# Kernel optimization log

Hardware: AMD Instinct MI355X
Metric: run time of the kernel (lower is better)

The kernel has to match this reference:

```python
import jax, jax.numpy as jnp
import numpy as np

EPS = 1e-8  # torch.cosine_similarity eps
TEMPERATURE = 1.0


def setup_inputs() -> dict:
    key = jax.random.key(0)
    ks = jax.random.split(key, 12)
    B = 16384
    inp = {
        "user_ids": jax.random.randint(ks[0], (B, 8), 0, 100000),
        "item_ids": jax.random.randint(ks[1], (B, 4), 0, 50000),
        "sample_weight": jax.random.uniform(ks[2], (B,), jnp.float32, 0.01, 1.0),
        "user_table": jax.random.normal(ks[3], (100000, 64), jnp.float32) * 0.05,
        "item_table": jax.random.normal(ks[4], (50000, 64), jnp.float32) * 0.05,
        "uW1": jax.random.normal(ks[5], (512, 256), jnp.float32) * 0.04,
        "ub1": jnp.zeros((256,), jnp.float32),
        "uW2": jax.random.normal(ks[6], (256, 128), jnp.float32) * 0.06,
        "ub2": jnp.zeros((128,), jnp.float32),
        "iW1": jax.random.normal(ks[7], (256, 256), jnp.float32) * 0.06,
        "ib1": jnp.zeros((256,), jnp.float32),
        "iW2": jax.random.normal(ks[8], (256, 128), jnp.float32) * 0.06,
        "ib2": jnp.zeros((128,), jnp.float32),
        "n_neg": 3,
    }
    return inp


def _tower(ids, table, W1, b1, W2, b2):
    # embedding lookup [B, F, D] -> concat -> [B, F*D], then 2-layer relu MLP
    B = ids.shape[0]
    e = table[ids].reshape(B, -1)
    h = jax.nn.relu(e @ W1 + b1)
    return jax.nn.relu(h @ W2 + b2)


def reference(user_ids, item_ids, sample_weight, user_table, item_table,
              uW1, ub1, uW2, ub2, iW1, ib1, iW2, ib2, n_neg):
    u = _tower(user_ids, user_table, uW1, ub1, uW2, ub2)  # [B, 128]
    v = _tower(item_ids, item_table, iW1, ib1, iW2, ib2)  # [B, 128]
    # cosine similarity per row (torch eps clamp on norms)
    un = jnp.maximum(jnp.linalg.norm(u, axis=1), EPS)
    vn = jnp.maximum(jnp.linalg.norm(v, axis=1), EPS)
    y = jnp.sum(u * v, axis=1) / (un * vn)
    # sampling-bias correction
    y = y - jnp.log(sample_weight)
    # vectorized wrap-around in-batch negative gather:
    # scores[i] = [y[i], y[(i+1)%B], ..., y[(i+n_neg)%B]]
    B = y.shape[0]
    idx = (jnp.arange(B)[:, None] + jnp.arange(n_neg + 1)[None, :]) % B
    scores = y[idx] / TEMPERATURE  # [B, 1+n_neg]
    return scores
```

## Files before the change

### kernel.cpp

```cpp
#include <hip/hip_runtime.h>
#include <math.h>

#define CEPS 1e-8f

typedef __attribute__((ext_vector_type(8))) short bf16x8;
typedef __attribute__((ext_vector_type(4))) float f32x4;
typedef __attribute__((ext_vector_type(4))) unsigned int u32x4;

__device__ __forceinline__ unsigned short f2bf(float f) {
    unsigned u = __builtin_bit_cast(unsigned, f);
    u += 0x7fffu + ((u >> 16) & 1u);
    return (unsigned short)(u >> 16);
}

__global__ __launch_bounds__(256)
void pack_all(const float* __restrict__ uW1, const float* __restrict__ uW2,
              const float* __restrict__ iW1, const float* __restrict__ iW2,
              unsigned short* __restrict__ o1, unsigned short* __restrict__ o2,
              unsigned short* __restrict__ o3, unsigned short* __restrict__ o4)
{
    int g = blockIdx.x * 256 + threadIdx.x;
    const float* src; unsigned short* dst; int N; int base;
    if (g < 16384)      { src = uW1; dst = o1; N = 256; base = 0;     }
    else if (g < 20480) { src = uW2; dst = o2; N = 128; base = 16384; }
    else if (g < 28672) { src = iW1; dst = o3; N = 256; base = 20480; }
    else                { src = iW2; dst = o4; N = 128; base = 28672; }
    int i = g - base;
    int kg = i / N, n = i - kg * N;
    unsigned short tmp[8];
    #pragma unroll
    for (int j = 0; j < 8; ++j)
        tmp[j] = f2bf(src[(kg * 8 + j) * N + n]);
    *reinterpret_cast<bf16x8*>(dst + ((size_t)i << 3)) =
        *reinterpret_cast<bf16x8*>(tmp);
}


template<int F>
__device__ __forceinline__ void stage_emb(const int* __restrict__ ids,
                                          const float* __restrict__ table,
                                          unsigned short* e_s, int row0, int tid)
{
    constexpr int FC = F * 8;
    constexpr int IT = (64 * FC) / 1024;
    int idv[IT];
    #pragma unroll
    for (int it = 0; it < IT; ++it) {
        int c = tid + it * 1024;
        int r = c / FC, f = (c % FC) >> 3;
        idv[it] = ids[(row0 + r) * F + f];
    }
    #pragma unroll
    for (int it = 0; it < IT; ++it) {
        int c = tid + it * 1024;
        int r = c / FC, rem = c % FC, ci = rem & 7;
        const float* src = table + (size_t)idv[it] * 64 + ci * 8;
        float4 aa = *reinterpret_cast<const float4*>(src);
        float4 bb = *reinterpret_cast<const float4*>(src + 4);
        u32x4 pk;
        pk.x = f2bf(aa.x) | ((unsigned)f2bf(aa.y) << 16);
        pk.y = f2bf(aa.z) | ((unsigned)f2bf(aa.w) << 16);
        pk.z = f2bf(bb.x) | ((unsigned)f2bf(bb.y) << 16);
        pk.w = f2bf(bb.z) | ((unsigned)f2bf(bb.w) << 16);
        int byte = r * (F * 128) + rem * 16;
        byte ^= (r & 7) << 4;
        *reinterpret_cast<u32x4*>(reinterpret_cast<char*>(e_s) + byte) = pk;
    }
}

template<int KB>
__device__ __forceinline__ bf16x8 loadA(const unsigned short* s, int ks, int m,
                                        int l15, int l4)
{
    int row = m * 16 + l15;
    int byte = row * (KB * 2) + ks * 64 + l4 * 16;
    byte ^= (row & 7) << 4;
    return *reinterpret_cast<const bf16x8*>(
               reinterpret_cast<const char*>(s) + byte);
}

template<int K1>
__device__ __forceinline__ void gemm1(
    const unsigned short* e_s, unsigned short* h_s,
    const unsigned short* __restrict__ W1p, const float* __restrict__ b1,
    int l15, int l4, int wl, const bf16x8* b0)
{
    constexpr int NKS = K1 / 32;
    const int colbase = wl * 32;
    f32x4 acc[4][2];
    #pragma unroll
    for (int m = 0; m < 4; ++m)
        #pragma unroll
        for (int n = 0; n < 2; ++n) acc[m][n] = (f32x4){0.f, 0.f, 0.f, 0.f};

    const unsigned short* Wbase = W1p + (((l4 * 256) + colbase + l15) << 3);
    bf16x8 aB[2][4], bB[2][2];
    bB[0][0] = b0[0];
    bB[0][1] = b0[1];
    #pragma unroll
    for (int m = 0; m < 4; ++m) aB[0][m] = loadA<K1>(e_s, 0, m, l15, l4);

    #pragma unroll
    for (int ks = 0; ks < NKS; ++ks) {
        const int cur = ks & 1, nxt = cur ^ 1;
        if (ks + 1 < NKS) {
            #pragma unroll
            for (int m = 0; m < 4; ++m)
                aB[nxt][m] = loadA<K1>(e_s, ks + 1, m, l15, l4);
            #pragma unroll
            for (int n = 0; n < 2; ++n)
                bB[nxt][n] = *reinterpret_cast<const bf16x8*>(
                                 Wbase + (ks + 1) * 8192 + (n << 7));
        }
        #pragma unroll
        for (int n = 0; n < 2; ++n)
            #pragma unroll
            for (int m = 0; m < 4; ++m)
                acc[m][n] = __builtin_amdgcn_mfma_f32_16x16x32_bf16(
                                aB[cur][m], bB[cur][n], acc[m][n], 0, 0, 0);
    }
    #pragma unroll
    for (int n = 0; n < 2; ++n) {
        int col = colbase + n * 16 + l15;
        float bias = b1[col];
        #pragma unroll
        for (int m = 0; m < 4; ++m)
            #pragma unroll
            for (int r = 0; r < 4; ++r) {
                int row = m * 16 + l4 * 4 + r;
                float v = acc[m][n][r] + bias;
                v = v > 0.f ? v : 0.f;
                int byte = (row * 256 + col) * 2;
                byte ^= (row & 7) << 4;
                *reinterpret_cast<unsigned short*>(
                    reinterpret_cast<char*>(h_s) + byte) = f2bf(v);
            }
    }
}

__device__ __forceinline__ void gemm2(
    const unsigned short* h_s, const unsigned short* __restrict__ W2p,
    f32x4 (&acc)[4], int l15, int l4, int wl, bf16x8 b0)
{
    const int col = wl * 16 + l15;
    #pragma unroll
    for (int m = 0; m < 4; ++m) acc[m] = (f32x4){0.f, 0.f, 0.f, 0.f};

    const unsigned short* Wbase = W2p + (((l4 * 128) + col) << 3);
    bf16x8 aB[2][4], bB[2];
    bB[0] = b0;
    #pragma unroll
    for (int m = 0; m < 4; ++m) aB[0][m] = loadA<256>(h_s, 0, m, l15, l4);

    #pragma unroll
    for (int ks = 0; ks < 8; ++ks) {
        const int cur = ks & 1, nxt = cur ^ 1;
        if (ks + 1 < 8) {
            #pragma unroll
            for (int m = 0; m < 4; ++m)
                aB[nxt][m] = loadA<256>(h_s, ks + 1, m, l15, l4);
            bB[nxt] = *reinterpret_cast<const bf16x8*>(Wbase + (ks + 1) * 4096);
        }
        #pragma unroll
        for (int m = 0; m < 4; ++m)
            acc[m] = __builtin_amdgcn_mfma_f32_16x16x32_bf16(
                         aB[cur][m], bB[cur], acc[m], 0, 0, 0);
    }
}

__global__ __launch_bounds__(1024)
void fused_sbc(const int* __restrict__ user_ids,  const int* __restrict__ item_ids,
               const float* __restrict__ user_table, const float* __restrict__ item_table,
               const unsigned short* __restrict__ uW1p, const float* __restrict__ ub1,
               const unsigned short* __restrict__ uW2p, const float* __restrict__ ub2,
               const unsigned short* __restrict__ iW1p, const float* __restrict__ ib1,
               const unsigned short* __restrict__ iW2p, const float* __restrict__ ib2,
               const float* __restrict__ sw, float* __restrict__ out,
               int B, int nn1)
{
    __shared__ __align__(16) unsigned short smem[81920];
    unsigned short* e_u = smem;
    unsigned short* e_i = smem + 32768;
    unsigned short* h_u = smem + 49152;
    unsigned short* h_i = smem + 65536;
    float* V_lds = reinterpret_cast<float*>(smem);
    float* red   = reinterpret_cast<float*>(smem + 32768);

    const int tid  = threadIdx.x;
    const int lane = tid & 63;
    const int w    = tid >> 6;
    const int l15  = lane & 15, l4 = lane >> 4;
    const int role = w >> 3;
    const int wl   = w & 7;
    const int row0 = blockIdx.x * 64;

    const unsigned short* W1sel = role ? iW1p : uW1p;
    const unsigned short* W2sel = role ? iW2p : uW2p;

    bf16x8 b0g1[2];
    {
        const unsigned short* base = W1sel + ((l4 * 256 + wl * 32 + l15) << 3);
        b0g1[0] = *reinterpret_cast<const bf16x8*>(base);
        b0g1[1] = *reinterpret_cast<const bf16x8*>(base + 128);
    }
    stage_emb<8>(user_ids, user_table, e_u, row0, tid);
    stage_emb<4>(item_ids, item_table, e_i, row0, tid);
    __syncthreads();

    if (role == 0) gemm1<512>(e_u, h_u, uW1p, ub1, l15, l4, wl, b0g1);
    else           gemm1<256>(e_i, h_i, iW1p, ib1, l15, l4, wl, b0g1);
    bf16x8 b0g2 = *reinterpret_cast<const bf16x8*>(
                      W2sel + ((l4 * 128 + wl * 16 + l15) << 3));
    __syncthreads();

    f32x4 acc2[4];
    if (role == 0) gemm2(h_u, uW2p, acc2, l15, l4, wl, b0g2);
    else           gemm2(h_i, iW2p, acc2, l15, l4, wl, b0g2);

    const int col = wl * 16 + l15;

    if (role == 1) {
        const float bv = ib2[col];
        float pv[16];
        #pragma unroll
        for (int m = 0; m < 4; ++m)
            #pragma unroll
            for (int r = 0; r < 4; ++r) {
                float vv = acc2[m][r] + bv;
                vv = vv > 0.f ? vv : 0.f;
                int row = m * 16 + l4 * 4 + r;
                V_lds[row * 132 + col] = vv;
                pv[m * 4 + r] = vv * vv;
            }
        #pragma unroll
        for (int off = 1; off < 16; off <<= 1)
            #pragma unroll
            for (int i = 0; i < 16; ++i)
                pv[i] += __shfl_xor(pv[i], off);
        if (l15 == 0) {
            #pragma unroll
            for (int m = 0; m < 4; ++m)
                #pragma unroll
                for (int r = 0; r < 4; ++r) {
                    int row = m * 16 + l4 * 4 + r;
                    red[(wl * 64 + row) * 3 + 2] = pv[m * 4 + r];
                }
        }
    }
    __syncthreads();

    if (role == 0) {
        const float bu = ub2[col];
        float pd[16], pu[16];
        #pragma unroll
        for (int m = 0; m < 4; ++m)
            #pragma unroll
            for (int r = 0; r < 4; ++r) {
                float uu = acc2[m][r] + bu;
                uu = uu > 0.f ? uu : 0.f;
                int row = m * 16 + l4 * 4 + r;
                float vv = V_lds[row * 132 + col];
                pd[m * 4 + r] = uu * vv;
                pu[m * 4 + r] = uu * uu;
            }
        #pragma unroll
        for (int off = 1; off < 16; off <<= 1)
            #pragma unroll
            for (int i = 0; i < 16; ++i) {
                pd[i] += __shfl_xor(pd[i], off);
                pu[i] += __shfl_xor(pu[i], off);
            }
        if (l15 == 0) {
            #pragma unroll
            for (int m = 0; m < 4; ++m)
                #pragma unroll
                for (int r = 0; r < 4; ++r) {
                    int row = m * 16 + l4 * 4 + r;
                    red[(wl * 64 + row) * 3 + 0] = pd[m * 4 + r];
                    red[(wl * 64 + row) * 3 + 1] = pu[m * 4 + r];
                }
        }
    }
    __syncthreads();

    if (tid < 64) {
        int row = tid;
        float d = 0.f, su = 0.f, sv = 0.f;
        #pragma unroll
        for (int cg = 0; cg < 8; ++cg) {
            d  += red[(cg * 64 + row) * 3 + 0];
            su += red[(cg * 64 + row) * 3 + 1];
            sv += red[(cg * 64 + row) * 3 + 2];
        }
        float un = fmaxf(sqrtf(su), CEPS);
        float vn = fmaxf(sqrtf(sv), CEPS);
        int grow = row0 + row;
        float yv = d / (un * vn) - logf(sw[grow]);
        for (int j = 0; j < nn1; ++j) {
            int idx = grow - j;
            if (idx < 0) idx += B;
            out[idx * nn1 + j] = yv;
        }
    }
}

extern "C" void kernel_launch(void* const* d_in, const int* in_sizes, int n_in,
                              void* d_out, int out_size, void* d_ws, size_t ws_size,
                              hipStream_t stream)
{
    const int*   user_ids   = (const int*)  d_in[0];
    const int*   item_ids   = (const int*)  d_in[1];
    const float* sw         = (const float*)d_in[2];
    const float* user_table = (const float*)d_in[3];
    const float* item_table = (const float*)d_in[4];
    const float* uW1        = (const float*)d_in[5];
    const float* ub1        = (const float*)d_in[6];
    const float* uW2        = (const float*)d_in[7];
    const float* ub2        = (const float*)d_in[8];
    const float* iW1        = (const float*)d_in[9];
    const float* ib1        = (const float*)d_in[10];
    const float* iW2        = (const float*)d_in[11];
    const float* ib2        = (const float*)d_in[12];

    const int B   = in_sizes[2];
    const int nn1 = out_size / B;

    unsigned short* wp   = (unsigned short*)d_ws;
    unsigned short* uW1p = wp;
    unsigned short* uW2p = wp + 131072;
    unsigned short* iW1p = wp + 163840;
    unsigned short* iW2p = wp + 229376;
    float* out = (float*)d_out;

    pack_all<<<128, 256, 0, stream>>>(uW1, uW2, iW1, iW2,
                                      uW1p, uW2p, iW1p, iW2p);
    fused_sbc<<<B / 64, 1024, 0, stream>>>(user_ids, item_ids,
                                           user_table, item_table,
                                           uW1p, ub1, uW2p, ub2,
                                           iW1p, ib1, iW2p, ib2,
                                           sw, out, B, nn1);
}
```

Measured before the change: 32.40 us.

## Swap MFMA operand roles, triple-buffer weight loads, vectorize epilogue reductions

Weights now feed the MFMA A operand and activations the B operand, so each lane's accumulator holds 4 consecutive output columns of one row. This lets the bias/ReLU epilogue write packed 8-byte bf16 stores and cuts the cosine reductions from 4-step 16-wide shuffles over 16 values to 2 shuffles over 4 values. Global weight fragments are prefetched two k-steps ahead with a 3-slot ring, MFMA blocks run under raised s_setprio, and launch bounds ask for 4 waves per SIMD. The V staging stride drops to 129. Risks are register pressure from the deeper prefetch under the tighter launch bound, and possible LDS bank conflicts in the new store pattern.

Result: faster. 28.56 us (-11.8%).

```diff
diff --git a/kernel.cpp b/kernel.cpp
--- a/kernel.cpp
+++ b/kernel.cpp
@@ -6,6 +6,7 @@
 typedef __attribute__((ext_vector_type(8))) short bf16x8;
 typedef __attribute__((ext_vector_type(4))) float f32x4;
 typedef __attribute__((ext_vector_type(4))) unsigned int u32x4;
+typedef __attribute__((ext_vector_type(2))) unsigned int u32x2;
 
 __device__ __forceinline__ unsigned short f2bf(float f) {
     unsigned u = __builtin_bit_cast(unsigned, f);
@@ -53,8 +54,8 @@
     #pragma unroll
     for (int it = 0; it < IT; ++it) {
         int c = tid + it * 1024;
-        int r = c / FC, rem = c % FC, ci = rem & 7;
-        const float* src = table + (size_t)idv[it] * 64 + ci * 8;
+        int r = c / FC, rem = c % FC;
+        const float* src = table + (size_t)idv[it] * 64 + (rem & 7) * 8;
         float4 aa = *reinterpret_cast<const float4*>(src);
         float4 bb = *reinterpret_cast<const float4*>(src + 4);
         u32x4 pk;
@@ -69,10 +70,10 @@
 }
 
 template<int KB>
-__device__ __forceinline__ bf16x8 loadA(const unsigned short* s, int ks, int m,
+__device__ __forceinline__ bf16x8 loadA(const unsigned short* s, int ks, int ni,
                                         int l15, int l4)
 {
-    int row = m * 16 + l15;
+    int row = ni * 16 + l15;
     int byte = row * (KB * 2) + ks * 64 + l4 * 16;
     byte ^= (row & 7) << 4;
     return *reinterpret_cast<const bf16x8*>(
@@ -83,92 +84,105 @@
 __device__ __forceinline__ void gemm1(
     const unsigned short* e_s, unsigned short* h_s,
     const unsigned short* __restrict__ W1p, const float* __restrict__ b1,
-    int l15, int l4, int wl, const bf16x8* b0)
+    int l15, int l4, int wl, const bf16x8* w0)
 {
     constexpr int NKS = K1 / 32;
-    const int colbase = wl * 32;
-    f32x4 acc[4][2];
-    #pragma unroll
-    for (int m = 0; m < 4; ++m)
-        #pragma unroll
-        for (int n = 0; n < 2; ++n) acc[m][n] = (f32x4){0.f, 0.f, 0.f, 0.f};
-
-    const unsigned short* Wbase = W1p + (((l4 * 256) + colbase + l15) << 3);
-    bf16x8 aB[2][4], bB[2][2];
-    bB[0][0] = b0[0];
-    bB[0][1] = b0[1];
-    #pragma unroll
-    for (int m = 0; m < 4; ++m) aB[0][m] = loadA<K1>(e_s, 0, m, l15, l4);
+    f32x4 acc[2][4];
+    #pragma unroll
+    for (int mi = 0; mi < 2; ++mi)
+        #pragma unroll
+        for (int ni = 0; ni < 4; ++ni) acc[mi][ni] = (f32x4){0.f, 0.f, 0.f, 0.f};
+
+    const unsigned short* Wbase = W1p + ((l4 * 256 + wl * 32 + l15) << 3);
+    bf16x8 wf[3][2], ef[2][4];
+    wf[0][0] = w0[0];
+    wf[0][1] = w0[1];
+    #pragma unroll
+    for (int mi = 0; mi < 2; ++mi)
+        wf[1][mi] = *reinterpret_cast<const bf16x8*>(Wbase + 8192 + (mi << 7));
+    #pragma unroll
+    for (int ni = 0; ni < 4; ++ni) ef[0][ni] = loadA<K1>(e_s, 0, ni, l15, l4);
 
     #pragma unroll
     for (int ks = 0; ks < NKS; ++ks) {
-        const int cur = ks & 1, nxt = cur ^ 1;
+        if (ks + 2 < NKS) {
+            #pragma unroll
+            for (int mi = 0; mi < 2; ++mi)
+                wf[(ks + 2) % 3][mi] = *reinterpret_cast<const bf16x8*>(
+                    Wbase + (ks + 2) * 8192 + (mi << 7));
+        }
         if (ks + 1 < NKS) {
             #pragma unroll
-            for (int m = 0; m < 4; ++m)
-                aB[nxt][m] = loadA<K1>(e_s, ks + 1, m, l15, l4);
-            #pragma unroll
-            for (int n = 0; n < 2; ++n)
-                bB[nxt][n] = *reinterpret_cast<const bf16x8*>(
-                                 Wbase + (ks + 1) * 8192 + (n << 7));
-        }
-        #pragma unroll
-        for (int n = 0; n < 2; ++n)
-            #pragma unroll
-            for (int m = 0; m < 4; ++m)
-                acc[m][n] = __builtin_amdgcn_mfma_f32_16x16x32_bf16(
-                                aB[cur][m], bB[cur][n], acc[m][n], 0, 0, 0);
-    }
-    #pragma unroll
-    for (int n = 0; n < 2; ++n) {
-        int col = colbase + n * 16 + l15;
-        float bias = b1[col];
-        #pragma unroll
-        for (int m = 0; m < 4; ++m)
-            #pragma unroll
-            for (int r = 0; r < 4; ++r) {
-                int row = m * 16 + l4 * 4 + r;
-                float v = acc[m][n][r] + bias;
-                v = v > 0.f ? v : 0.f;
-                int byte = (row * 256 + col) * 2;
-                byte ^= (row & 7) << 4;
-                *reinterpret_cast<unsigned short*>(
-                    reinterpret_cast<char*>(h_s) + byte) = f2bf(v);
-            }
+            for (int ni = 0; ni < 4; ++ni)
+                ef[(ks + 1) & 1][ni] = loadA<K1>(e_s, ks + 1, ni, l15, l4);
+        }
+        __builtin_amdgcn_s_setprio(1);
+        #pragma unroll
+        for (int mi = 0; mi < 2; ++mi)
+            #pragma unroll
+            for (int ni = 0; ni < 4; ++ni)
+                acc[mi][ni] = __builtin_amdgcn_mfma_f32_16x16x32_bf16(
+                                  wf[ks % 3][mi], ef[ks & 1][ni], acc[mi][ni], 0, 0, 0);
+        __builtin_amdgcn_s_setprio(0);
+    }
+    float4 bias[2];
+    bias[0] = *reinterpret_cast<const float4*>(&b1[wl * 32 + l4 * 4]);
+    bias[1] = *reinterpret_cast<const float4*>(&b1[wl * 32 + 16 + l4 * 4]);
+    #pragma unroll
+    for (int mi = 0; mi < 2; ++mi) {
+        const float4 bb = bias[mi];
+        #pragma unroll
+        for (int ni = 0; ni < 4; ++ni) {
+            float v0 = acc[mi][ni][0] + bb.x; v0 = v0 > 0.f ? v0 : 0.f;
+            float v1 = acc[mi][ni][1] + bb.y; v1 = v1 > 0.f ? v1 : 0.f;
+            float v2 = acc[mi][ni][2] + bb.z; v2 = v2 > 0.f ? v2 : 0.f;
+            float v3 = acc[mi][ni][3] + bb.w; v3 = v3 > 0.f ? v3 : 0.f;
+            u32x2 d;
+            d.x = f2bf(v0) | ((unsigned)f2bf(v1) << 16);
+            d.y = f2bf(v2) | ((unsigned)f2bf(v3) << 16);
+            int row = ni * 16 + l15;
+            int w0c = wl * 32 + mi * 16 + l4 * 4;
+            int byte = (row * 256 + w0c) * 2;
+            byte ^= (row & 7) << 4;
+            *reinterpret_cast<u32x2*>(reinterpret_cast<char*>(h_s) + byte) = d;
+        }
     }
 }
 
 __device__ __forceinline__ void gemm2(
     const unsigned short* h_s, const unsigned short* __restrict__ W2p,
-    f32x4 (&acc)[4], int l15, int l4, int wl, bf16x8 b0)
-{
-    const int col = wl * 16 + l15;
-    #pragma unroll
-    for (int m = 0; m < 4; ++m) acc[m] = (f32x4){0.f, 0.f, 0.f, 0.f};
-
-    const unsigned short* Wbase = W2p + (((l4 * 128) + col) << 3);
-    bf16x8 aB[2][4], bB[2];
-    bB[0] = b0;
-    #pragma unroll
-    for (int m = 0; m < 4; ++m) aB[0][m] = loadA<256>(h_s, 0, m, l15, l4);
+    f32x4 (&acc)[4], int l15, int l4, int wl, bf16x8 w0)
+{
+    #pragma unroll
+    for (int ni = 0; ni < 4; ++ni) acc[ni] = (f32x4){0.f, 0.f, 0.f, 0.f};
+
+    const unsigned short* Wbase = W2p + ((l4 * 128 + wl * 16 + l15) << 3);
+    bf16x8 wf[3], hf[2][4];
+    wf[0] = w0;
+    wf[1] = *reinterpret_cast<const bf16x8*>(Wbase + 4096);
+    #pragma unroll
+    for (int ni = 0; ni < 4; ++ni) hf[0][ni] = loadA<256>(h_s, 0, ni, l15, l4);
 
     #pragma unroll
     for (int ks = 0; ks < 8; ++ks) {
-        const int cur = ks & 1, nxt = cur ^ 1;
+        if (ks + 2 < 8)
+            wf[(ks + 2) % 3] = *reinterpret_cast<const bf16x8*>(
+                                   Wbase + (ks + 2) * 4096);
         if (ks + 1 < 8) {
             #pragma unroll
-            for (int m = 0; m < 4; ++m)
-                aB[nxt][m] = loadA<256>(h_s, ks + 1, m, l15, l4);
-            bB[nxt] = *reinterpret_cast<const bf16x8*>(Wbase + (ks + 1) * 4096);
-        }
-        #pragma unroll
-        for (int m = 0; m < 4; ++m)
-            acc[m] = __builtin_amdgcn_mfma_f32_16x16x32_bf16(
-                         aB[cur][m], bB[cur], acc[m], 0, 0, 0);
-    }
-}
-
-__global__ __launch_bounds__(1024)
+            for (int ni = 0; ni < 4; ++ni)
+                hf[(ks + 1) & 1][ni] = loadA<256>(h_s, ks + 1, ni, l15, l4);
+        }
+        __builtin_amdgcn_s_setprio(1);
+        #pragma unroll
+        for (int ni = 0; ni < 4; ++ni)
+            acc[ni] = __builtin_amdgcn_mfma_f32_16x16x32_bf16(
+                          wf[ks % 3], hf[ks & 1][ni], acc[ni], 0, 0, 0);
+        __builtin_amdgcn_s_setprio(0);
+    }
+}
+
+__global__ __launch_bounds__(1024, 4)
 void fused_sbc(const int* __restrict__ user_ids,  const int* __restrict__ item_ids,
                const float* __restrict__ user_table, const float* __restrict__ item_table,
                const unsigned short* __restrict__ uW1p, const float* __restrict__ ub1,
@@ -197,88 +211,87 @@
     const unsigned short* W1sel = role ? iW1p : uW1p;
     const unsigned short* W2sel = role ? iW2p : uW2p;
 
-    bf16x8 b0g1[2];
+    bf16x8 w0g1[2];
     {
         const unsigned short* base = W1sel + ((l4 * 256 + wl * 32 + l15) << 3);
-        b0g1[0] = *reinterpret_cast<const bf16x8*>(base);
-        b0g1[1] = *reinterpret_cast<const bf16x8*>(base + 128);
+        w0g1[0] = *reinterpret_cast<const bf16x8*>(base);
+        w0g1[1] = *reinterpret_cast<const bf16x8*>(base + 128);
     }
     stage_emb<8>(user_ids, user_table, e_u, row0, tid);
     stage_emb<4>(item_ids, item_table, e_i, row0, tid);
     __syncthreads();
 
-    if (role == 0) gemm1<512>(e_u, h_u, uW1p, ub1, l15, l4, wl, b0g1);
-    else           gemm1<256>(e_i, h_i, iW1p, ib1, l15, l4, wl, b0g1);
-    bf16x8 b0g2 = *reinterpret_cast<const bf16x8*>(
+    if (role == 0) gemm1<512>(e_u, h_u, uW1p, ub1, l15, l4, wl, w0g1);
+    else           gemm1<256>(e_i, h_i, iW1p, ib1, l15, l4, wl, w0g1);
+    bf16x8 w0g2 = *reinterpret_cast<const bf16x8*>(
                       W2sel + ((l4 * 128 + wl * 16 + l15) << 3));
     __syncthreads();
 
     f32x4 acc2[4];
-    if (role == 0) gemm2(h_u, uW2p, acc2, l15, l4, wl, b0g2);
-    else           gemm2(h_i, iW2p, acc2, l15, l4, wl, b0g2);
-
-    const int col = wl * 16 + l15;
+    if (role == 0) gemm2(h_u, uW2p, acc2, l15, l4, wl, w0g2);
+    else           gemm2(h_i, iW2p, acc2, l15, l4, wl, w0g2);
+
+    const int colb = wl * 16 + l4 * 4;
 
     if (role == 1) {
-        const float bv = ib2[col];
-        float pv[16];
-        #pragma unroll
-        for (int m = 0; m < 4; ++m)
-            #pragma unroll
-            for (int r = 0; r < 4; ++r) {
-                float vv = acc2[m][r] + bv;
-                vv = vv > 0.f ? vv : 0.f;
-                int row = m * 16 + l4 * 4 + r;
-                V_lds[row * 132 + col] = vv;
-                pv[m * 4 + r] = vv * vv;
+        const float4 bv = *reinterpret_cast<const float4*>(&ib2[colb]);
+        float pv[4];
+        #pragma unroll
+        for (int ni = 0; ni < 4; ++ni) {
+            int row = ni * 16 + l15;
+            float v0 = acc2[ni][0] + bv.x; v0 = v0 > 0.f ? v0 : 0.f;
+            float v1 = acc2[ni][1] + bv.y; v1 = v1 > 0.f ? v1 : 0.f;
+            float v2 = acc2[ni][2] + bv.z; v2 = v2 > 0.f ? v2 : 0.f;
+            float v3 = acc2[ni][3] + bv.w; v3 = v3 > 0.f ? v3 : 0.f;
+            V_lds[row * 129 + colb + 0] = v0;
+            V_lds[row * 129 + colb + 1] = v1;
+            V_lds[row * 129 + colb + 2] = v2;
+            V_lds[row * 129 + colb + 3] = v3;
+            pv[ni] = v0 * v0 + v1 * v1 + v2 * v2 + v3 * v3;
+        }
+        #pragma unroll
+        for (int ni = 0; ni < 4; ++ni) {
+            pv[ni] += __shfl_xor(pv[ni], 16);
+            pv[ni] += __shfl_xor(pv[ni], 32);
+        }
+        if (l4 == 0) {
+            #pragma unroll
+            for (int ni = 0; ni < 4; ++ni)
+                red[(wl * 64 + ni * 16 + l15) * 3 + 2] = pv[ni];
+        }
+    }
+    __syncthreads();
+
+    if (role == 0) {
+        const float4 bu = *reinterpret_cast<const float4*>(&ub2[colb]);
+        float pd[4], pu[4];
+        #pragma unroll
+        for (int ni = 0; ni < 4; ++ni) {
+            int row = ni * 16 + l15;
+            float u0 = acc2[ni][0] + bu.x; u0 = u0 > 0.f ? u0 : 0.f;
+            float u1 = acc2[ni][1] + bu.y; u1 = u1 > 0.f ? u1 : 0.f;
+            float u2 = acc2[ni][2] + bu.z; u2 = u2 > 0.f ? u2 : 0.f;
+            float u3 = acc2[ni][3] + bu.w; u3 = u3 > 0.f ? u3 : 0.f;
+            float v0 = V_lds[row * 129 + colb + 0];
+            float v1 = V_lds[row * 129 + colb + 1];
+            float v2 = V_lds[row * 129 + colb + 2];
+            float v3 = V_lds[row * 129 + colb + 3];
+            pd[ni] = u0 * v0 + u1 * v1 + u2 * v2 + u3 * v3;
+            pu[ni] = u0 * u0 + u1 * u1 + u2 * u2 + u3 * u3;
+        }
+        #pragma unroll
+        for (int ni = 0; ni < 4; ++ni) {
+            pd[ni] += __shfl_xor(pd[ni], 16);
+            pd[ni] += __shfl_xor(pd[ni], 32);
+            pu[ni] += __shfl_xor(pu[ni], 16);
+            pu[ni] += __shfl_xor(pu[ni], 32);
+        }
+        if (l4 == 0) {
+            #pragma unroll
+            for (int ni = 0; ni < 4; ++ni) {
+                red[(wl * 64 + ni * 16 + l15) * 3 + 0] = pd[ni];
+                red[(wl * 64 + ni * 16 + l15) * 3 + 1] = pu[ni];
             }
-        #pragma unroll
-        for (int off = 1; off < 16; off <<= 1)
-            #pragma unroll
-            for (int i = 0; i < 16; ++i)
-                pv[i] += __shfl_xor(pv[i], off);
-        if (l15 == 0) {
-            #pragma unroll
-            for (int m = 0; m < 4; ++m)
-                #pragma unroll
-                for (int r = 0; r < 4; ++r) {
-                    int row = m * 16 + l4 * 4 + r;
-                    red[(wl * 64 + row) * 3 + 2] = pv[m * 4 + r];
-                }
-        }
-    }
-    __syncthreads();
-
-    if (role == 0) {
-        const float bu = ub2[col];
-        float pd[16], pu[16];
-        #pragma unroll
-        for (int m = 0; m < 4; ++m)
-            #pragma unroll
-            for (int r = 0; r < 4; ++r) {
-                float uu = acc2[m][r] + bu;
-                uu = uu > 0.f ? uu : 0.f;
-                int row = m * 16 + l4 * 4 + r;
-                float vv = V_lds[row * 132 + col];
-                pd[m * 4 + r] = uu * vv;
-                pu[m * 4 + r] = uu * uu;
-            }
-        #pragma unroll
-        for (int off = 1; off < 16; off <<= 1)
-            #pragma unroll
-            for (int i = 0; i < 16; ++i) {
-                pd[i] += __shfl_xor(pd[i], off);
-                pu[i] += __shfl_xor(pu[i], off);
-            }
-        if (l15 == 0) {
-            #pragma unroll
-            for (int m = 0; m < 4; ++m)
-                #pragma unroll
-                for (int r = 0; r < 4; ++r) {
-                    int row = m * 16 + l4 * 4 + r;
-                    red[(wl * 64 + row) * 3 + 0] = pd[m * 4 + r];
-                    red[(wl * 64 + row) * 3 + 1] = pu[m * 4 + r];
-                }
         }
     }
     __syncthreads();
```
